# Kernel tuning notes

Measured on AMD Instinct MI355X. Metric: run time of the kernel, lower is better.

Reference implementation:

```python
import jax, jax.numpy as jnp
import numpy as np

N = 100000      # nodes
E = 1600000     # edges
F_IN = 128
F_HID = 128
F_OUT = 40
BN_EPS = 1e-5


def gcn_layer(x, W, b, src, dst):
    # PyG GCNConv with default gcn_norm: add self-loops, symmetric deg^-1/2 norm.
    h = x @ W                                   # [N, F_out] dense transform first (F_out <= F_in friendly)
    loop = jnp.arange(N)
    s = jnp.concatenate([src, loop])            # [E+N] sources incl. self-loops
    d = jnp.concatenate([dst, loop])            # [E+N] targets incl. self-loops
    deg = jax.ops.segment_sum(jnp.ones(s.shape, dtype=h.dtype), d, num_segments=N)
    dinv = jnp.where(deg > 0, jax.lax.rsqrt(deg), jnp.zeros((), h.dtype))
    norm = dinv[s] * dinv[d]                    # [E+N]
    out = jax.ops.segment_sum(h[s] * norm[:, None], d, num_segments=N)
    return out + b


def setup_inputs() -> dict:
    key = jax.random.key(0)
    ks = jax.random.split(key, 8)
    x = jax.random.normal(ks[0], (N, F_IN), dtype=jnp.float32)
    edge_src = jax.random.randint(ks[1], (E,), 0, N)
    edge_dst = jax.random.randint(ks[2], (E,), 0, N)
    W1 = jax.random.normal(ks[3], (F_IN, F_HID), dtype=jnp.float32) * (1.0 / np.sqrt(F_IN))
    b1 = jnp.zeros((F_HID,), dtype=jnp.float32)
    gamma = jnp.ones((F_HID,), dtype=jnp.float32)
    beta = jnp.zeros((F_HID,), dtype=jnp.float32)
    W2 = jax.random.normal(ks[4], (F_HID, F_OUT), dtype=jnp.float32) * (1.0 / np.sqrt(F_HID))
    b2 = jnp.zeros((F_OUT,), dtype=jnp.float32)
    return {"x": x, "W1": W1, "b1": b1, "gamma": gamma, "beta": beta,
            "W2": W2, "b2": b2, "edge_src": edge_src, "edge_dst": edge_dst}


def reference(x, W1, b1, gamma, beta, W2, b2, edge_src, edge_dst):
    h = gcn_layer(x, W1, b1, edge_src, edge_dst)            # GCNConv 1
    mean = jnp.mean(h, axis=0)                               # BatchNorm1d (batch stats, deterministic)
    var = jnp.mean(jnp.square(h - mean), axis=0)
    h = (h - mean) * jax.lax.rsqrt(var + BN_EPS) * gamma + beta
    h = jax.nn.relu(h)                                       # ReLU; dropout is identity (eval/deterministic)
    h = gcn_layer(h, W2, b2, edge_src, edge_dst)            # GCNConv 2
    return jax.nn.log_softmax(h, axis=1)
```

## Files before the change

kernel.cpp:

```cpp
#include <hip/hip_runtime.h>
#include <cstdint>
#include <cstddef>

constexpr int N_NODES = 100000;
constexpr int N_EDGES = 1600000;
constexpr int F_IN   = 128;
constexpr int F_HID  = 128;
constexpr int F_OUT  = 40;
constexpr float BN_EPS = 1e-5f;

constexpr int NBUCK  = 196;
constexpr int ECHUNK = 4096;
constexpr int NCHUNK = (N_EDGES + ECHUNK - 1) / ECHUNK;
constexpr int BCAP   = 16384;

typedef unsigned int uint;
typedef unsigned short ushort;
typedef __attribute__((ext_vector_type(8))) short short8v;
typedef __attribute__((ext_vector_type(4))) float f32x4;

__device__ inline uint bf16_rne(float f) {
    uint u = __float_as_uint(f);
    return (u + 0x7fffu + ((u >> 16) & 1u)) >> 16;
}
__device__ inline float bf_lo(uint u) { return __uint_as_float(u << 16); }
__device__ inline float bf_hi(uint u) { return __uint_as_float(u & 0xffff0000u); }

__global__ __launch_bounds__(256) void k_wcast(const float* __restrict__ W1,
                                               const float* __restrict__ W2,
                                               ushort* __restrict__ w1b,
                                               ushort* __restrict__ w2b,
                                               int* __restrict__ gfill,
                                               float* __restrict__ bnsum,
                                               float* __restrict__ bnsq) {
    int i = blockIdx.x * 256 + threadIdx.x;
    if (i < NBUCK) gfill[i] = 0;
    if (i < 128) { bnsum[i] = 0.f; bnsq[i] = 0.f; }
    if (i < 128 * 128) {
        int n = i >> 7, k = i & 127;
        w1b[i] = (ushort)bf16_rne(W1[k * 128 + n]);
    }
    if (i < 48 * 128) {
        int c = i >> 7, k = i & 127;
        w2b[i] = (c < F_OUT) ? (ushort)bf16_rne(W2[k * F_OUT + c]) : (ushort)0;
    }
}

__global__ __launch_bounds__(256) void k_part(const int* __restrict__ src,
                                              const int* __restrict__ dst,
                                              int* __restrict__ gfill,
                                              uint* __restrict__ ebuf) {
    __shared__ uint pk[ECHUNK];
    __shared__ uint gd[ECHUNK];
    __shared__ int hist[NBUCK], loff[NBUCK], gpos[NBUCK], lfill[NBUCK];
    __shared__ int sc[256];
    int t = threadIdx.x;
    for (int i = t; i < NBUCK; i += 256) { hist[i] = 0; lfill[i] = 0; }
    __syncthreads();
    int base = blockIdx.x * ECHUNK;
    int n = min(ECHUNK, N_EDGES - base);
    for (int i = t; i < n; i += 256)
        atomicAdd(&hist[dst[base + i] >> 9], 1);
    __syncthreads();
    int c = (t < NBUCK) ? hist[t] : 0;
    sc[t] = c;
    __syncthreads();
    #pragma unroll
    for (int o = 1; o < 256; o <<= 1) {
        int v = (t >= o) ? sc[t - o] : 0;
        __syncthreads();
        sc[t] += v;
        __syncthreads();
    }
    if (t < NBUCK) {
        loff[t] = sc[t] - c;
        gpos[t] = c ? atomicAdd(&gfill[t], c) : 0;
    }
    __syncthreads();
    for (int i = t; i < n; i += 256) {
        int d = dst[base + i];
        int s2 = src[base + i];
        int b = d >> 9;
        int lp = atomicAdd(&lfill[b], 1);
        int idx = loff[b] + lp;
        int off = gpos[b] + lp;
        pk[idx] = (uint)s2 | ((uint)(d & 511) << 17);
        gd[idx] = (off < BCAP) ? (uint)(b * BCAP + off) : 0xFFFFFFFFu;
    }
    __syncthreads();
    for (int i = t; i < n; i += 256) {
        uint g = gd[i];
        if (g != 0xFFFFFFFFu) ebuf[g] = pk[i];
    }
}

__global__ __launch_bounds__(256) void k_csr(const uint* __restrict__ ebuf,
                                             const int* __restrict__ gfill,
                                             int* __restrict__ rowptr,
                                             int* __restrict__ rowend,
                                             float* __restrict__ dinv,
                                             int* __restrict__ colidx) {
    __shared__ int hist[512];
    __shared__ int lptr[512];
    int t = threadIdx.x;
    int b = blockIdx.x;
    int v0 = b << 9;
    int e0 = b * BCAP;
    int m = min(gfill[b], BCAP);
    for (int i = t; i < 512; i += 256) hist[i] = 0;
    __syncthreads();
    for (int i = t; i < m; i += 256)
        atomicAdd(&hist[ebuf[e0 + i] >> 17], 1);
    __syncthreads();
    if (t < 64) {
        int run = 0;
        #pragma unroll
        for (int j = 0; j < 8; ++j) { lptr[8 * t + j] = run; run += hist[8 * t + j]; }
        int inc = run;
        #pragma unroll
        for (int o = 1; o < 64; o <<= 1) {
            int u = __shfl_up(inc, o);
            if (t >= o) inc += u;
        }
        int excl = inc - run;
        #pragma unroll
        for (int j = 0; j < 8; ++j) lptr[8 * t + j] += excl;
    }
    __syncthreads();
    for (int i = t; i < 512; i += 256) {
        int v = v0 + i;
        if (v < N_NODES) {
            int beg = e0 + lptr[i];
            rowptr[v] = beg;
            rowend[v] = beg + hist[i];
            dinv[v] = rsqrtf((float)(hist[i] + 1));
        }
    }
    __syncthreads();
    for (int i = t; i < 512; i += 256) hist[i] = 0;
    __syncthreads();
    for (int i = t; i < m; i += 256) {
        uint p = ebuf[e0 + i];
        int lr = (int)(p >> 17);
        int lp = atomicAdd(&hist[lr], 1);
        colidx[e0 + lptr[lr] + lp] = (int)(p & 0x1FFFFu);
    }
}

__global__ __launch_bounds__(256) void k_gemm1(const float* __restrict__ x,
                                               const ushort* __restrict__ w1b,
                                               const float* __restrict__ dinv,
                                               uint* __restrict__ h1b) {
    __shared__ float sm[64 * 132];
    int wid = threadIdx.x >> 6, lane = threadIdx.x & 63;
    int li = lane & 15, kg = lane >> 4;
    int row = blockIdx.x * 64 + wid * 16 + li;
    int rc = min(row, N_NODES - 1);
    const float* xr = x + (size_t)rc * 128;
    f32x4 acc[8] = {};
    #pragma unroll
    for (int kk = 0; kk < 4; ++kk) {
        int k0 = kk * 32 + kg * 8;
        float4 xv0 = *(const float4*)(xr + k0);
        float4 xv1 = *(const float4*)(xr + k0 + 4);
        short8v a;
        a[0] = (short)bf16_rne(xv0.x); a[1] = (short)bf16_rne(xv0.y);
        a[2] = (short)bf16_rne(xv0.z); a[3] = (short)bf16_rne(xv0.w);
        a[4] = (short)bf16_rne(xv1.x); a[5] = (short)bf16_rne(xv1.y);
        a[6] = (short)bf16_rne(xv1.z); a[7] = (short)bf16_rne(xv1.w);
        #pragma unroll
        for (int n = 0; n < 8; ++n) {
            short8v b = *(const short8v*)(w1b + (n * 16 + li) * 128 + k0);
            acc[n] = __builtin_amdgcn_mfma_f32_16x16x32_bf16(a, b, acc[n], 0, 0, 0);
        }
    }
    #pragma unroll
    for (int n = 0; n < 8; ++n)
        #pragma unroll
        for (int j = 0; j < 4; ++j)
            sm[(wid * 16 + kg * 4 + j) * 132 + n * 16 + li] = acc[n][j];
    __syncthreads();
    int rr = threadIdx.x >> 2, cb = (threadIdx.x & 3) * 32;
    int grow = blockIdx.x * 64 + rr;
    if (grow < N_NODES) {
        float dv = dinv[grow];
        const float4* sp4 = (const float4*)(sm + rr * 132 + cb);
        uint4 ov[4];
        #pragma unroll
        for (int q = 0; q < 4; ++q) {
            float4 e0 = sp4[2 * q], e1 = sp4[2 * q + 1];
            ov[q].x = bf16_rne(e0.x * dv) | (bf16_rne(e0.y * dv) << 16);
            ov[q].y = bf16_rne(e0.z * dv) | (bf16_rne(e0.w * dv) << 16);
            ov[q].z = bf16_rne(e1.x * dv) | (bf16_rne(e1.y * dv) << 16);
            ov[q].w = bf16_rne(e1.z * dv) | (bf16_rne(e1.w * dv) << 16);
        }
        uint4* dst = (uint4*)(h1b + (size_t)grow * 64 + cb / 2);
        #pragma unroll
        for (int q = 0; q < 4; ++q) dst[q] = ov[q];
    }
}

__global__ __launch_bounds__(256) void k_agg1(const uint* __restrict__ h1b,
                                              const int* __restrict__ rowptr,
                                              const int* __restrict__ rowend,
                                              const int* __restrict__ colidx,
                                              const float* __restrict__ dinv,
                                              const float* __restrict__ b1,
                                              uint* __restrict__ out1b) {
    const uint4* h1b4 = (const uint4*)h1b;
    int v = __builtin_amdgcn_readfirstlane(blockIdx.x * 4 + (threadIdx.x >> 6));
    if (v >= N_NODES) return;
    int lane = threadIdx.x & 63;
    int g = lane >> 4, c = lane & 15;
    int beg = rowptr[v], end = rowend[v];
    float a0 = 0, a1 = 0, a2 = 0, a3 = 0, a4 = 0, a5 = 0, a6 = 0, a7 = 0;
    #define ACC8(u) { a0 += bf_lo(u.x); a1 += bf_hi(u.x); a2 += bf_lo(u.y); a3 += bf_hi(u.y); \
                      a4 += bf_lo(u.z); a5 += bf_hi(u.z); a6 += bf_lo(u.w); a7 += bf_hi(u.w); }
    if (g == 0) {
        uint4 us = h1b4[(size_t)v * 16 + c];
        ACC8(us);
    }
    int p = beg + g;
    for (; p + 12 < end; p += 16) {
        int s0 = colidx[p], s1 = colidx[p + 4], s2 = colidx[p + 8], s3 = colidx[p + 12];
        uint4 u0 = h1b4[(size_t)s0 * 16 + c];
        uint4 u1 = h1b4[(size_t)s1 * 16 + c];
        uint4 u2 = h1b4[(size_t)s2 * 16 + c];
        uint4 u3 = h1b4[(size_t)s3 * 16 + c];
        ACC8(u0); ACC8(u1); ACC8(u2); ACC8(u3);
    }
    for (; p < end; p += 4) {
        uint4 u = h1b4[(size_t)colidx[p] * 16 + c];
        ACC8(u);
    }
    #undef ACC8
    a0 += __shfl_xor(a0, 16); a0 += __shfl_xor(a0, 32);
    a1 += __shfl_xor(a1, 16); a1 += __shfl_xor(a1, 32);
    a2 += __shfl_xor(a2, 16); a2 += __shfl_xor(a2, 32);
    a3 += __shfl_xor(a3, 16); a3 += __shfl_xor(a3, 32);
    a4 += __shfl_xor(a4, 16); a4 += __shfl_xor(a4, 32);
    a5 += __shfl_xor(a5, 16); a5 += __shfl_xor(a5, 32);
    a6 += __shfl_xor(a6, 16); a6 += __shfl_xor(a6, 32);
    a7 += __shfl_xor(a7, 16); a7 += __shfl_xor(a7, 32);
    if (g == 0) {
        float dv = dinv[v];
        const float* bp = b1 + 8 * c;
        float o0 = fmaf(dv, a0, bp[0]), o1 = fmaf(dv, a1, bp[1]);
        float o2 = fmaf(dv, a2, bp[2]), o3 = fmaf(dv, a3, bp[3]);
        float o4 = fmaf(dv, a4, bp[4]), o5 = fmaf(dv, a5, bp[5]);
        float o6 = fmaf(dv, a6, bp[6]), o7 = fmaf(dv, a7, bp[7]);
        uint4 ov;
        ov.x = bf16_rne(o0) | (bf16_rne(o1) << 16);
        ov.y = bf16_rne(o2) | (bf16_rne(o3) << 16);
        ov.z = bf16_rne(o4) | (bf16_rne(o5) << 16);
        ov.w = bf16_rne(o6) | (bf16_rne(o7) << 16);
        *(uint4*)(out1b + (size_t)v * 64 + 4 * c) = ov;
    }
}

__global__ __launch_bounds__(256) void k_bnstats(const uint* __restrict__ out1b,
                                                 float* __restrict__ sum,
                                                 float* __restrict__ sumsq) {
    int t = threadIdx.x;
    int f = t & 63;
    int r = blockIdx.x * 4 + (t >> 6);
    float s0 = 0, ss0 = 0, s1 = 0, ss1 = 0;
    for (; r < N_NODES; r += gridDim.x * 4) {
        uint u = out1b[(size_t)r * 64 + f];
        float a = bf_lo(u), b = bf_hi(u);
        s0 += a; ss0 += a * a;
        s1 += b; ss1 += b * b;
    }
    __shared__ float ls[256][4];
    ls[t][0] = s0; ls[t][1] = ss0; ls[t][2] = s1; ls[t][3] = ss1;
    __syncthreads();
    if (t < 64) {
        float A = ls[t][0] + ls[t + 64][0] + ls[t + 128][0] + ls[t + 192][0];
        float B = ls[t][1] + ls[t + 64][1] + ls[t + 128][1] + ls[t + 192][1];
        float C = ls[t][2] + ls[t + 64][2] + ls[t + 128][2] + ls[t + 192][2];
        float D = ls[t][3] + ls[t + 64][3] + ls[t + 128][3] + ls[t + 192][3];
        atomicAdd(&sum[2 * f], A);
        atomicAdd(&sumsq[2 * f], B);
        atomicAdd(&sum[2 * f + 1], C);
        atomicAdd(&sumsq[2 * f + 1], D);
    }
}

__global__ __launch_bounds__(256) void k_gemm2(const uint* __restrict__ out1b,
                                               const ushort* __restrict__ w2b,
                                               const float* __restrict__ bnsum,
                                               const float* __restrict__ bnsq,
                                               const float* __restrict__ gamma,
                                               const float* __restrict__ beta,
                                               const float* __restrict__ dinv,
                                               uint* __restrict__ h2f) {
    __shared__ float sm[64 * 52];
    __shared__ float scs[128], shs[128];
    if (threadIdx.x < 128) {
        int f = threadIdx.x;
        float mean = bnsum[f] * (1.f / N_NODES);
        float var = bnsq[f] * (1.f / N_NODES) - mean * mean;
        float rstd = rsqrtf(var + BN_EPS);
        float sc = gamma[f] * rstd;
        scs[f] = sc;
        shs[f] = beta[f] - mean * sc;
    }
    __syncthreads();
    int wid = threadIdx.x >> 6, lane = threadIdx.x & 63;
    int li = lane & 15, kg = lane >> 4;
    int row = blockIdx.x * 64 + wid * 16 + li;
    int rc = min(row, N_NODES - 1);
    const uint* xr = out1b + (size_t)rc * 64;
    f32x4 acc[3] = {};
    #pragma unroll
    for (int kk = 0; kk < 4; ++kk) {
        int k0 = kk * 32 + kg * 8;
        uint4 uv = *(const uint4*)(xr + k0 / 2);
        float4 sc0 = *(const float4*)(scs + k0);
        float4 sc1 = *(const float4*)(scs + k0 + 4);
        float4 sh0 = *(const float4*)(shs + k0);
        float4 sh1 = *(const float4*)(shs + k0 + 4);
        float e0 = fmaxf(fmaf(bf_lo(uv.x), sc0.x, sh0.x), 0.f);
        float e1 = fmaxf(fmaf(bf_hi(uv.x), sc0.y, sh0.y), 0.f);
        float e2 = fmaxf(fmaf(bf_lo(uv.y), sc0.z, sh0.z), 0.f);
        float e3 = fmaxf(fmaf(bf_hi(uv.y), sc0.w, sh0.w), 0.f);
        float e4 = fmaxf(fmaf(bf_lo(uv.z), sc1.x, sh1.x), 0.f);
        float e5 = fmaxf(fmaf(bf_hi(uv.z), sc1.y, sh1.y), 0.f);
        float e6 = fmaxf(fmaf(bf_lo(uv.w), sc1.z, sh1.z), 0.f);
        float e7 = fmaxf(fmaf(bf_hi(uv.w), sc1.w, sh1.w), 0.f);
        short8v a;
        a[0] = (short)bf16_rne(e0); a[1] = (short)bf16_rne(e1);
        a[2] = (short)bf16_rne(e2); a[3] = (short)bf16_rne(e3);
        a[4] = (short)bf16_rne(e4); a[5] = (short)bf16_rne(e5);
        a[6] = (short)bf16_rne(e6); a[7] = (short)bf16_rne(e7);
        #pragma unroll
        for (int n = 0; n < 3; ++n) {
            short8v b = *(const short8v*)(w2b + (n * 16 + li) * 128 + k0);
            acc[n] = __builtin_amdgcn_mfma_f32_16x16x32_bf16(a, b, acc[n], 0, 0, 0);
        }
    }
    #pragma unroll
    for (int n = 0; n < 3; ++n)
        #pragma unroll
        for (int j = 0; j < 4; ++j)
            sm[(wid * 16 + kg * 4 + j) * 52 + n * 16 + li] = acc[n][j];
    __syncthreads();
    int rr = threadIdx.x;
    int grow = blockIdx.x * 64 + rr;
    if (rr < 64 && grow < N_NODES) {
        float dv = dinv[grow];
        const float* sp = sm + rr * 52;
        uint o[10];
        #pragma unroll
        for (int i = 0; i < 10; ++i) {
            int p = 0;
            p = __builtin_amdgcn_cvt_pk_fp8_f32(sp[4 * i] * dv,     sp[4 * i + 1] * dv, p, false);
            p = __builtin_amdgcn_cvt_pk_fp8_f32(sp[4 * i + 2] * dv, sp[4 * i + 3] * dv, p, true);
            o[i] = (uint)p;
        }
        uint4* dst = (uint4*)(h2f + (size_t)grow * 16);
        dst[0] = make_uint4(o[0], o[1], o[2], o[3]);
        dst[1] = make_uint4(o[4], o[5], o[6], o[7]);
        *(uint2*)(h2f + (size_t)grow * 16 + 8) = make_uint2(o[8], o[9]);
    }
}

__global__ __launch_bounds__(256) void k_agg2(const uint* __restrict__ h2f,
                                              const int* __restrict__ rowptr,
                                              const int* __restrict__ rowend,
                                              const int* __restrict__ colidx,
                                              const float* __restrict__ dinv,
                                              const float* __restrict__ b2,
                                              float* __restrict__ out) {
    __shared__ float sm[4][64][4];
    int wid = threadIdx.x >> 6;
    int v = __builtin_amdgcn_readfirstlane(blockIdx.x * 4 + wid);
    if (v >= N_NODES) return;
    int lane = threadIdx.x & 63;
    int g = lane / 10;
    int c = lane - g * 10;
    bool act = g < 6;
    int beg = rowptr[v], end = rowend[v];
    float a0 = 0, a1 = 0, a2 = 0, a3 = 0;
    #define ACC4(u) { auto lo = __builtin_amdgcn_cvt_pk_f32_fp8((int)(u), false); \
                      auto hi = __builtin_amdgcn_cvt_pk_f32_fp8((int)(u), true);  \
                      a0 += lo[0]; a1 += lo[1]; a2 += hi[0]; a3 += hi[1]; }
    if (act) {
        if (g == 0) {
            uint u = h2f[(size_t)v * 16 + c];
            ACC4(u);
        }
        int p = beg + g;
        for (; p + 18 < end; p += 24) {
            int s0 = colidx[p], s1 = colidx[p + 6], s2 = colidx[p + 12], s3 = colidx[p + 18];
            uint u0 = h2f[(size_t)s0 * 16 + c];
            uint u1 = h2f[(size_t)s1 * 16 + c];
            uint u2 = h2f[(size_t)s2 * 16 + c];
            uint u3 = h2f[(size_t)s3 * 16 + c];
            ACC4(u0); ACC4(u1); ACC4(u2); ACC4(u3);
        }
        for (; p < end; p += 6) {
            uint u = h2f[(size_t)colidx[p] * 16 + c];
            ACC4(u);
        }
    }
    #undef ACC4
    float4* slot = (float4*)&sm[wid][lane][0];
    *slot = make_float4(a0, a1, a2, a3);
    asm volatile("s_waitcnt lgkmcnt(0)" ::: "memory");
    __builtin_amdgcn_sched_barrier(0);
    float z = -1e30f;
    if (lane < F_OUT) {
        int cc = lane >> 2, jj = lane & 3;
        float s = sm[wid][cc][jj]      + sm[wid][10 + cc][jj] + sm[wid][20 + cc][jj]
                + sm[wid][30 + cc][jj] + sm[wid][40 + cc][jj] + sm[wid][50 + cc][jj];
        z = fmaf(dinv[v], s, b2[lane]);
    }
    float m = z;
    #pragma unroll
    for (int off = 32; off; off >>= 1) m = fmaxf(m, __shfl_xor(m, off));
    float e = (lane < F_OUT) ? __expf(z - m) : 0.f;
    float ssum = e;
    #pragma unroll
    for (int off = 32; off; off >>= 1) ssum += __shfl_xor(ssum, off);
    if (lane < F_OUT) out[(size_t)v * F_OUT + lane] = z - m - __logf(ssum);
}

extern "C" void kernel_launch(void* const* d_in, const int* in_sizes, int n_in,
                              void* d_out, int out_size, void* d_ws, size_t ws_size,
                              hipStream_t stream) {
    const float* x     = (const float*)d_in[0];
    const float* W1    = (const float*)d_in[1];
    const float* b1    = (const float*)d_in[2];
    const float* gamma = (const float*)d_in[3];
    const float* beta  = (const float*)d_in[4];
    const float* W2    = (const float*)d_in[5];
    const float* b2    = (const float*)d_in[6];
    const int* esrc    = (const int*)d_in[7];
    const int* edst    = (const int*)d_in[8];
    float* out         = (float*)d_out;

    char* w = (char*)d_ws;
    size_t off = 0;
    auto alloc = [&](size_t bytes) -> void* {
        void* p = w + off;
        off = (off + bytes + 255) & ~(size_t)255;
        return p;
    };
    int*   gfill  = (int*)alloc(NBUCK * 4);
    int*   rowptr = (int*)alloc(N_NODES * 4);
    int*   rowend = (int*)alloc(N_NODES * 4);
    float* dinv   = (float*)alloc(N_NODES * 4);
    int*   colidx = (int*)alloc((size_t)NBUCK * BCAP * 4);
    uint*  h1b    = (uint*)alloc((size_t)N_NODES * 64 * 4);
    uint*  out1b  = (uint*)alloc((size_t)N_NODES * 64 * 4);
    uint*  h2f    = (uint*)alloc((size_t)N_NODES * 16 * 4);
    ushort* w1b   = (ushort*)alloc(128 * 128 * 2);
    ushort* w2b   = (ushort*)alloc(48 * 128 * 2);
    float* bnsum  = (float*)alloc(128 * 4);
    float* bnsq   = (float*)alloc(128 * 4);
    uint*  ebuf   = h1b;

    (void)ws_size; (void)in_sizes; (void)n_in; (void)out_size;

    k_wcast<<<64, 256, 0, stream>>>(W1, W2, w1b, w2b, gfill, bnsum, bnsq);

    k_part <<<NCHUNK, 256, 0, stream>>>(esrc, edst, gfill, ebuf);
    k_csr  <<<NBUCK, 256, 0, stream>>>(ebuf, gfill, rowptr, rowend, dinv, colidx);

    k_gemm1<<<(N_NODES + 63) / 64, 256, 0, stream>>>(x, w1b, dinv, h1b);
    k_agg1<<<(N_NODES + 3) / 4, 256, 0, stream>>>(h1b, rowptr, rowend, colidx, dinv, b1, out1b);

    k_bnstats<<<512, 256, 0, stream>>>(out1b, bnsum, bnsq);

    k_gemm2<<<(N_NODES + 63) / 64, 256, 0, stream>>>(out1b, w2b, bnsum, bnsq, gamma, beta, dinv, h2f);
    k_agg2<<<(N_NODES + 3) / 4, 256, 0, stream>>>(h2f, rowptr, rowend, colidx, dinv, b2, out);
}
```

Before: 255.3 us.

## Use 16-byte vector gathers in layer-2 aggregation with cross-lane reduction

Measured after the change: 292.4 us. 14.5% more time.

```diff
diff --git a/kernel.cpp b/kernel.cpp
--- a/kernel.cpp
+++ b/kernel.cpp
@@ -350,7 +350,7 @@
     if (rr < 64 && grow < N_NODES) {
         float dv = dinv[grow];
         const float* sp = sm + rr * 52;
-        uint o[10];
+        uint o[16];
         #pragma unroll
         for (int i = 0; i < 10; ++i) {
             int p = 0;
@@ -358,64 +358,63 @@
             p = __builtin_amdgcn_cvt_pk_fp8_f32(sp[4 * i + 2] * dv, sp[4 * i + 3] * dv, p, true);
             o[i] = (uint)p;
         }
+        #pragma unroll
+        for (int i = 10; i < 16; ++i) o[i] = 0u;
         uint4* dst = (uint4*)(h2f + (size_t)grow * 16);
-        dst[0] = make_uint4(o[0], o[1], o[2], o[3]);
-        dst[1] = make_uint4(o[4], o[5], o[6], o[7]);
-        *(uint2*)(h2f + (size_t)grow * 16 + 8) = make_uint2(o[8], o[9]);
-    }
-}
-
-__global__ __launch_bounds__(256) void k_agg2(const uint* __restrict__ h2f,
+        #pragma unroll
+        for (int q = 0; q < 4; ++q)
+            dst[q] = make_uint4(o[4 * q], o[4 * q + 1], o[4 * q + 2], o[4 * q + 3]);
+    }
+}
+
+__global__ __launch_bounds__(256) void k_agg2(const uint4* __restrict__ h2f4,
                                               const int* __restrict__ rowptr,
                                               const int* __restrict__ rowend,
                                               const int* __restrict__ colidx,
                                               const float* __restrict__ dinv,
                                               const float* __restrict__ b2,
                                               float* __restrict__ out) {
-    __shared__ float sm[4][64][4];
+    __shared__ float sm[4][68];
     int wid = threadIdx.x >> 6;
     int v = __builtin_amdgcn_readfirstlane(blockIdx.x * 4 + wid);
     if (v >= N_NODES) return;
     int lane = threadIdx.x & 63;
-    int g = lane / 10;
-    int c = lane - g * 10;
-    bool act = g < 6;
+    int g = lane >> 2, c = lane & 3;
     int beg = rowptr[v], end = rowend[v];
-    float a0 = 0, a1 = 0, a2 = 0, a3 = 0;
-    #define ACC4(u) { auto lo = __builtin_amdgcn_cvt_pk_f32_fp8((int)(u), false); \
-                      auto hi = __builtin_amdgcn_cvt_pk_f32_fp8((int)(u), true);  \
-                      a0 += lo[0]; a1 += lo[1]; a2 += hi[0]; a3 += hi[1]; }
-    if (act) {
-        if (g == 0) {
-            uint u = h2f[(size_t)v * 16 + c];
-            ACC4(u);
-        }
-        int p = beg + g;
-        for (; p + 18 < end; p += 24) {
-            int s0 = colidx[p], s1 = colidx[p + 6], s2 = colidx[p + 12], s3 = colidx[p + 18];
-            uint u0 = h2f[(size_t)s0 * 16 + c];
-            uint u1 = h2f[(size_t)s1 * 16 + c];
-            uint u2 = h2f[(size_t)s2 * 16 + c];
-            uint u3 = h2f[(size_t)s3 * 16 + c];
-            ACC4(u0); ACC4(u1); ACC4(u2); ACC4(u3);
-        }
-        for (; p < end; p += 6) {
-            uint u = h2f[(size_t)colidx[p] * 16 + c];
-            ACC4(u);
-        }
-    }
-    #undef ACC4
-    float4* slot = (float4*)&sm[wid][lane][0];
-    *slot = make_float4(a0, a1, a2, a3);
+    float a[16] = {};
+    #define ACC16(u) { \
+        { auto t2 = __builtin_amdgcn_cvt_pk_f32_fp8((int)(u.x), false); a[0]  += t2[0]; a[1]  += t2[1]; } \
+        { auto t2 = __builtin_amdgcn_cvt_pk_f32_fp8((int)(u.x), true);  a[2]  += t2[0]; a[3]  += t2[1]; } \
+        { auto t2 = __builtin_amdgcn_cvt_pk_f32_fp8((int)(u.y), false); a[4]  += t2[0]; a[5]  += t2[1]; } \
+        { auto t2 = __builtin_amdgcn_cvt_pk_f32_fp8((int)(u.y), true);  a[6]  += t2[0]; a[7]  += t2[1]; } \
+        { auto t2 = __builtin_amdgcn_cvt_pk_f32_fp8((int)(u.z), false); a[8]  += t2[0]; a[9]  += t2[1]; } \
+        { auto t2 = __builtin_amdgcn_cvt_pk_f32_fp8((int)(u.z), true);  a[10] += t2[0]; a[11] += t2[1]; } \
+        { auto t2 = __builtin_amdgcn_cvt_pk_f32_fp8((int)(u.w), false); a[12] += t2[0]; a[13] += t2[1]; } \
+        { auto t2 = __builtin_amdgcn_cvt_pk_f32_fp8((int)(u.w), true);  a[14] += t2[0]; a[15] += t2[1]; } }
+    if (g == 15) {
+        uint4 u = h2f4[(size_t)v * 4 + c];
+        ACC16(u);
+    }
+    for (int p = beg + g; p < end; p += 16) {
+        int s = colidx[p];
+        uint4 u = h2f4[(size_t)s * 4 + c];
+        ACC16(u);
+    }
+    #undef ACC16
+    #pragma unroll
+    for (int j = 0; j < 16; ++j) {
+        a[j] += __shfl_xor(a[j], 4);
+        a[j] += __shfl_xor(a[j], 8);
+        a[j] += __shfl_xor(a[j], 16);
+        a[j] += __shfl_xor(a[j], 32);
+    }
+    if (g == 0) {
+        #pragma unroll
+        for (int j = 0; j < 16; ++j) sm[wid][c * 16 + j] = a[j];
+    }
     asm volatile("s_waitcnt lgkmcnt(0)" ::: "memory");
     __builtin_amdgcn_sched_barrier(0);
-    float z = -1e30f;
-    if (lane < F_OUT) {
-        int cc = lane >> 2, jj = lane & 3;
-        float s = sm[wid][cc][jj]      + sm[wid][10 + cc][jj] + sm[wid][20 + cc][jj]
-                + sm[wid][30 + cc][jj] + sm[wid][40 + cc][jj] + sm[wid][50 + cc][jj];
-        z = fmaf(dinv[v], s, b2[lane]);
-    }
+    float z = (lane < F_OUT) ? fmaf(dinv[v], sm[wid][lane], b2[lane]) : -1e30f;
     float m = z;
     #pragma unroll
     for (int off = 32; off; off >>= 1) m = fmaxf(m, __shfl_xor(m, off));
@@ -474,5 +473,5 @@
     k_bnstats<<<512, 256, 0, stream>>>(out1b, bnsum, bnsq);
 
     k_gemm2<<<(N_NODES + 63) / 64, 256, 0, stream>>>(out1b, w2b, bnsum, bnsq, gamma, beta, dinv, h2f);
-    k_agg2<<<(N_NODES + 3) / 4, 256, 0, stream>>>(h2f, rowptr, rowend, colidx, dinv, b2, out);
-}
+    k_agg2<<<(N_NODES + 3) / 4, 256, 0, stream>>>((const uint4*)h2f, rowptr, rowend, colidx, dinv, b2, out);
+}
```
